# Kernel optimization log

Hardware: AMD Instinct MI355X
Metric: run time of the kernel (lower is better)

Reference implementation:

```python
import jax, jax.numpy as jnp
import numpy as np

B, N, D, K = 32, 196, 1024, 512  # batch, tokens (14x14), feature dim, prototypes
EPS = 1e-8  # torch F.cosine_similarity default eps


def setup_inputs() -> dict:
    key = jax.random.key(0)
    ks = jax.random.split(key, 8)
    z = jax.random.normal(ks[0], (B, N, D), jnp.float32)
    prototypes = jax.random.normal(ks[1], (K, D), jnp.float32)  # nn.Parameter(randn)
    gate_w = jax.random.normal(ks[2], (2 * D, D), jnp.float32) * 0.02  # Linear(2D->D), stored [in,out]
    gate_b = jnp.zeros((D,), jnp.float32)
    dec_w = jax.random.normal(ks[3], (D, 7 * 7 * 512), jnp.float32) * 0.02
    dec_b = jnp.zeros((7 * 7 * 512,), jnp.float32)
    ct1_w = jax.random.normal(ks[4], (512, 256, 4, 4), jnp.float32) * 0.02  # torch [in,out,kh,kw]
    ct1_b = jnp.zeros((256,), jnp.float32)
    ct2_w = jax.random.normal(ks[5], (256, 3, 4, 4), jnp.float32) * 0.02
    ct2_b = jnp.zeros((3,), jnp.float32)
    return dict(z=z, prototypes=prototypes, gate_w=gate_w, gate_b=gate_b,
                dec_w=dec_w, dec_b=dec_b, ct1_w=ct1_w, ct1_b=ct1_b,
                ct2_w=ct2_w, ct2_b=ct2_b)


def _conv_transpose(x, w, b):
    # ConvTranspose2d(k=4, stride=2, pad=1) == conv with lhs_dilation=2,
    # padding k-1-pad=2, spatially-flipped kernel, torch weight layout [in,out,kh,kw] -> IOHW.
    wf = jnp.flip(w, (2, 3))
    y = jax.lax.conv_general_dilated(
        x, wf, window_strides=(1, 1), padding=((2, 2), (2, 2)),
        lhs_dilation=(2, 2), dimension_numbers=("NCHW", "IOHW", "NCHW"))
    return y + b[None, :, None, None]


def reference(z, prototypes, gate_w, gate_b, dec_w, dec_b, ct1_w, ct1_b, ct2_w, ct2_b):
    # MemoryBank: cosine similarity of every token against every prototype
    zn = jnp.linalg.norm(z, axis=-1, keepdims=True)            # [B,N,1]
    pn = jnp.linalg.norm(prototypes, axis=-1)                  # [K]
    dots = jnp.einsum('bnd,kd->bnk', z, prototypes)            # [B,N,K]
    sim = dots / jnp.maximum(zn * pn[None, None, :], EPS)
    attn = jax.nn.softmax(sim, axis=-1)                        # [B,N,K]
    z_hat = jnp.einsum('bnk,kd->bnd', attn, prototypes)        # [B,N,D]
    # GatedFusion: sigmoid gate over concat(z, z_hat)
    gate = jax.nn.sigmoid(jnp.concatenate([z, z_hat], axis=-1) @ gate_w + gate_b)
    z_fused = gate * z + (1.0 - gate) * z_hat                  # [B,N,D]
    # Decoder (original reshape is shape-inconsistent; pool tokens -> [B,D])
    pooled = z_fused.mean(axis=1)                              # [B,D]
    h = (pooled @ dec_w + dec_b).reshape(-1, 512, 7, 7)
    h = jax.nn.relu(_conv_transpose(h, ct1_w, ct1_b))          # [B,256,14,14]
    x_recon = _conv_transpose(h, ct2_w, ct2_b)                 # [B,3,28,28]
    return x_recon, attn
```

## Files before the change

### kernel.cpp

```cpp
#include <hip/hip_runtime.h>
#include <cstdint>
#include <cstddef>
#include <cmath>

#define EPS_COS 1e-8f

typedef unsigned short u16;
typedef __attribute__((ext_vector_type(8))) short short8v;
typedef __attribute__((ext_vector_type(4))) short short4v;
typedef __attribute__((ext_vector_type(4))) float f32x4;

__device__ __forceinline__ u16 f2bf(float x) {
    unsigned int u = __float_as_uint(x);
    return (u16)((u + 0x7FFFu + ((u >> 16) & 1u)) >> 16);
}
__device__ __forceinline__ float bf2f(u16 h) {
    return __uint_as_float(((unsigned int)h) << 16);
}

__global__ __launch_bounds__(256) void norm_cvt_kernel(const float* __restrict__ src,
                                                       u16* __restrict__ dst, int dstStride,
                                                       float* __restrict__ norms) {
    int r = blockIdx.x;
    int t = threadIdx.x;
    const float4 v = *reinterpret_cast<const float4*>(&src[(size_t)r * 1024 + t * 4]);
    short4v o;
    o[0] = f2bf(v.x); o[1] = f2bf(v.y); o[2] = f2bf(v.z); o[3] = f2bf(v.w);
    *reinterpret_cast<short4v*>(&dst[(size_t)r * dstStride + t * 4]) = o;
    float ss = v.x * v.x + v.y * v.y + v.z * v.z + v.w * v.w;
#pragma unroll
    for (int off = 32; off > 0; off >>= 1) ss += __shfl_down(ss, off);
    __shared__ float red[4];
    int wave = t >> 6, lane = t & 63;
    if (lane == 0) red[wave] = ss;
    __syncthreads();
    if (t == 0) norms[r] = sqrtf(red[0] + red[1] + red[2] + red[3]);
}

__global__ __launch_bounds__(256) void transpose_cvt_kernel(const float* __restrict__ src,
                                                            u16* __restrict__ dst,
                                                            int R, int C) {
    __shared__ float tile[64][65];
    int c0 = blockIdx.x * 64, r0 = blockIdx.y * 64;
    int t = threadIdx.x;
#pragma unroll
    for (int j = 0; j < 16; ++j) {
        int idx = j * 256 + t;
        int r = idx >> 6, c = idx & 63;
        tile[r][c] = src[(size_t)(r0 + r) * C + c0 + c];
    }
    __syncthreads();
#pragma unroll
    for (int j = 0; j < 16; ++j) {
        int idx = j * 256 + t;
        int c = idx >> 6, r = idx & 63;
        dst[(size_t)(c0 + c) * R + r0 + r] = f2bf(tile[r][c]);
    }
}

__global__ __launch_bounds__(256) void prep_kernel(u16* __restrict__ hp,
                                                   const float* __restrict__ ct1w,
                                                   u16* __restrict__ wt,
                                                   const float* __restrict__ ct2w,
                                                   u16* __restrict__ wpad,
                                                   float* __restrict__ pooled) {
    int idx = blockIdx.x * 256 + threadIdx.x;
    if (idx < 165888) {
        short8v zv = {0, 0, 0, 0, 0, 0, 0, 0};
        *reinterpret_cast<short8v*>(hp + (size_t)idx * 8) = zv;
    } else if (idx < 165888 + 131072) {
        int i = idx - 165888;
        int oc = i & 255, ic = i >> 8;
        float v[16];
#pragma unroll
        for (int j = 0; j < 16; ++j) v[j] = ct1w[(size_t)i * 16 + j];
#pragma unroll
        for (int pp = 0; pp < 4; ++pp) {
            int py = pp >> 1, px = pp & 1;
#pragma unroll
            for (int tap = 0; tap < 4; ++tap) {
                int ty = tap >> 1, tx = tap & 1;
                int ky = (1 - py) + 2 * ty;
                int kx = (1 - px) + 2 * tx;
                wt[((size_t)(pp * 256 + oc)) * 2048 + ic * 4 + tap] = f2bf(v[ky * 4 + kx]);
            }
        }
    } else if (idx < 165888 + 131072 + 16384) {
        int i = idx - 165888 - 131072;
        int ic = i & 255;
        int col = i >> 8;
        float v = 0.0f;
        if (col < 48) {
            int kx = col & 3, ky = (col >> 2) & 3, oc = col >> 4;
            v = ct2w[((size_t)ic * 3 + oc) * 16 + ky * 4 + kx];
        }
        wpad[i] = f2bf(v);
    } else {
        int i = idx - 165888 - 131072 - 16384;
        *reinterpret_cast<f32x4*>(pooled + (size_t)i * 4) = (f32x4){0.f, 0.f, 0.f, 0.f};
    }
}

template <int FM, int FN, int EPI, bool SWZ>
__global__ __launch_bounds__(256) void mfma_gemm_kernel(
    const u16* __restrict__ A, int sA, size_t zsA,
    const u16* __restrict__ B, int sB, size_t zsB,
    int M, int N, int K,
    float* __restrict__ Cf,
    u16* __restrict__ Cb, int sCb,
    const float* __restrict__ bias,
    const u16* __restrict__ zbf,
    const u16* __restrict__ zhbf, int szh,
    float* __restrict__ outf) {
    constexpr int BM = FM * 32, BN = FN * 32;
    constexpr int NA = BM / 32;
    constexpr int NB = BN / 32;
    __shared__ __align__(16) u16 As[BM * 64];
    __shared__ __align__(16) u16 Bs[BN * 64];
    int bx = blockIdx.x, by = blockIdx.y;
    if (SWZ) {
        int gx = gridDim.x;
        int nwg = gx * gridDim.y;
        int lb = by * gx + bx;
        int flat = (lb & 7) * (nwg >> 3) + (lb >> 3);
        bx = flat % gx;
        by = flat / gx;
    }
    A += (size_t)blockIdx.z * zsA;
    B += (size_t)blockIdx.z * zsB;
    const int t = threadIdx.x;
    const int lane = t & 63;
    const int wid = t >> 6;
    const int wm = wid >> 1, wn = wid & 1;
    const int m0 = bx * BM, n0 = by * BN;
    const int g = lane >> 4, lr = lane & 15;

    f32x4 acc[FM][FN];
#pragma unroll
    for (int i = 0; i < FM; ++i)
#pragma unroll
        for (int j = 0; j < FN; ++j) acc[i][j] = (f32x4){0.f, 0.f, 0.f, 0.f};

    short8v ra[NA], rb[NB];
#pragma unroll
    for (int j = 0; j < NA; ++j) {
        int c = j * 256 + t, row = c >> 3, ck = c & 7;
        ra[j] = *reinterpret_cast<const short8v*>(A + (size_t)(m0 + row) * sA + ck * 8);
    }
#pragma unroll
    for (int j = 0; j < NB; ++j) {
        int c = j * 256 + t, row = c >> 3, ck = c & 7;
        rb[j] = *reinterpret_cast<const short8v*>(B + (size_t)(n0 + row) * sB + ck * 8);
    }

    for (int k0 = 0; k0 < K; k0 += 64) {
        __syncthreads();
#pragma unroll
        for (int j = 0; j < NA; ++j) {
            int c = j * 256 + t, row = c >> 3, ck = c & 7;
            *reinterpret_cast<short8v*>(As + row * 64 + ((ck ^ (row & 7)) << 3)) = ra[j];
        }
#pragma unroll
        for (int j = 0; j < NB; ++j) {
            int c = j * 256 + t, row = c >> 3, ck = c & 7;
            *reinterpret_cast<short8v*>(Bs + row * 64 + ((ck ^ (row & 7)) << 3)) = rb[j];
        }
        __syncthreads();
        if (k0 + 64 < K) {
#pragma unroll
            for (int j = 0; j < NA; ++j) {
                int c = j * 256 + t, row = c >> 3, ck = c & 7;
                ra[j] = *reinterpret_cast<const short8v*>(A + (size_t)(m0 + row) * sA + k0 + 64 + ck * 8);
            }
#pragma unroll
            for (int j = 0; j < NB; ++j) {
                int c = j * 256 + t, row = c >> 3, ck = c & 7;
                rb[j] = *reinterpret_cast<const short8v*>(B + (size_t)(n0 + row) * sB + k0 + 64 + ck * 8);
            }
        }
#pragma unroll
        for (int kk = 0; kk < 2; ++kk) {
            short8v af[FM], bfr[FN];
#pragma unroll
            for (int fm = 0; fm < FM; ++fm) {
                int row = wm * (FM * 16) + fm * 16 + lr;
                int rc = (kk * 4 + g) ^ (row & 7);
                af[fm] = *reinterpret_cast<const short8v*>(As + row * 64 + rc * 8);
            }
#pragma unroll
            for (int fn = 0; fn < FN; ++fn) {
                int col = wn * (FN * 16) + fn * 16 + lr;
                int rc = (kk * 4 + g) ^ (col & 7);
                bfr[fn] = *reinterpret_cast<const short8v*>(Bs + col * 64 + rc * 8);
            }
#pragma unroll
            for (int fm = 0; fm < FM; ++fm)
#pragma unroll
                for (int fn = 0; fn < FN; ++fn)
                    acc[fm][fn] = __builtin_amdgcn_mfma_f32_16x16x32_bf16(
                        af[fm], bfr[fn], acc[fm][fn], 0, 0, 0);
        }
    }

    if (EPI == 2) {
#pragma unroll
        for (int fn = 0; fn < FN; ++fn) {
            int col = n0 + wn * (FN * 16) + fn * 16 + lr;
            int base = m0 + wm * (FM * 16) + g * 4;
            int b0 = base / 196;
            float p0 = 0.f, p1 = 0.f;
#pragma unroll
            for (int fm = 0; fm < FM; ++fm) {
#pragma unroll
                for (int r = 0; r < 4; ++r) {
                    int row = base + fm * 16 + r;
                    float v = acc[fm][fn][r];
                    float gs = 1.0f / (1.0f + __expf(-(v + bias[col])));
                    float zv = bf2f(zbf[(size_t)row * szh + col]);
                    float zh = bf2f(zhbf[(size_t)row * szh + col]);
                    float fused = gs * zv + (1.0f - gs) * zh;
                    bool same = (row / 196) == b0;
                    p0 += same ? fused : 0.f;
                    p1 += same ? 0.f : fused;
                }
            }
            atomicAdd(&outf[(size_t)b0 * 1024 + col], p0);
            if (p1 != 0.f) atomicAdd(&outf[(size_t)(b0 + 1) * 1024 + col], p1);
        }
    } else {
#pragma unroll
        for (int fm = 0; fm < FM; ++fm) {
#pragma unroll
            for (int fn = 0; fn < FN; ++fn) {
#pragma unroll
                for (int r = 0; r < 4; ++r) {
                    int row = m0 + wm * (FM * 16) + fm * 16 + g * 4 + r;
                    int col = n0 + wn * (FN * 16) + fn * 16 + lr;
                    float v = acc[fm][fn][r];
                    if (EPI == 0) {
                        Cf[(size_t)row * N + col] = v;
                    } else if (EPI == 1) {
                        Cb[(size_t)row * sCb + col] = f2bf(v);
                    } else {
                        if (row < 1568) {
                            float vv = fmaxf(v + bias[col], 0.0f);
                            int bb = row / 49, ss = row - bb * 49;
                            Cb[(((size_t)bb * 4 + blockIdx.z) * 49 + ss) * 256 + col] = f2bf(vv);
                        }
                    }
                }
            }
        }
    }
}

__global__ __launch_bounds__(256) void softmax_kernel(const float* __restrict__ dots,
                                                      const float* __restrict__ zn,
                                                      const float* __restrict__ pn,
                                                      float* __restrict__ attn,
                                                      u16* __restrict__ attn_bf) {
    int m = blockIdx.x;
    int t = threadIdx.x;
    float zm = zn[m];
    float d0 = dots[(size_t)m * 512 + t];
    float d1 = dots[(size_t)m * 512 + t + 256];
    float v0 = d0 / fmaxf(zm * pn[t], EPS_COS);
    float v1 = d1 / fmaxf(zm * pn[t + 256], EPS_COS);
    float mx = fmaxf(v0, v1);
#pragma unroll
    for (int off = 32; off > 0; off >>= 1) mx = fmaxf(mx, __shfl_down(mx, off));
    __shared__ float red[8];
    int wave = t >> 6, lane = t & 63;
    if (lane == 0) red[wave] = mx;
    __syncthreads();
    if (t == 0) red[4] = fmaxf(fmaxf(red[0], red[1]), fmaxf(red[2], red[3]));
    __syncthreads();
    mx = red[4];
    float e0 = expf(v0 - mx), e1 = expf(v1 - mx);
    float s = e0 + e1;
#pragma unroll
    for (int off = 32; off > 0; off >>= 1) s += __shfl_down(s, off);
    if (lane == 0) red[wave] = s;
    __syncthreads();
    if (t == 0) red[5] = 1.0f / (red[0] + red[1] + red[2] + red[3]);
    __syncthreads();
    float r = red[5];
    float a0 = e0 * r, a1 = e1 * r;
    attn[(size_t)m * 512 + t] = a0;
    attn[(size_t)m * 512 + t + 256] = a1;
    attn_bf[(size_t)m * 512 + t] = f2bf(a0);
    attn_bf[(size_t)m * 512 + t + 256] = f2bf(a1);
}

#define DEC_KC 64
__global__ __launch_bounds__(256) void dec_split_kernel(const float* __restrict__ pooled,
                                                        const float* __restrict__ dec_w,
                                                        float* __restrict__ partial) {
    const int t = threadIdx.x;
    const int lane = t & 63;
    const int wv = t >> 6;
    const int c = blockIdx.x * 256 + lane * 4;
    const int kc = blockIdx.y;
    __shared__ float pl[32][DEC_KC];
    for (int i = t; i < 32 * DEC_KC; i += 256) {
        int b = i >> 6, kk = i & (DEC_KC - 1);
        pl[b][kk] = pooled[(size_t)b * 1024 + kc * DEC_KC + kk] * (1.0f / 196.0f);
    }
    __syncthreads();
    f32x4 acc[8];
#pragma unroll
    for (int j = 0; j < 8; ++j) acc[j] = (f32x4){0.f, 0.f, 0.f, 0.f};
    const float* wp = dec_w + (size_t)(kc * DEC_KC) * 25088 + c;
#pragma unroll 8
    for (int k = 0; k < DEC_KC; ++k) {
        f32x4 w4 = *reinterpret_cast<const f32x4*>(wp + (size_t)k * 25088);
#pragma unroll
        for (int j = 0; j < 8; ++j) {
            float pv = pl[wv * 8 + j][k];
            acc[j].x = fmaf(pv, w4.x, acc[j].x);
            acc[j].y = fmaf(pv, w4.y, acc[j].y);
            acc[j].z = fmaf(pv, w4.z, acc[j].z);
            acc[j].w = fmaf(pv, w4.w, acc[j].w);
        }
    }
#pragma unroll
    for (int j = 0; j < 8; ++j) {
        int b = wv * 8 + j;
        *reinterpret_cast<f32x4*>(partial + ((size_t)kc * 32 + b) * 25088 + c) = acc[j];
    }
}

__global__ __launch_bounds__(256) void dec_reduce_kernel(const float* __restrict__ partial,
                                                         const float* __restrict__ dec_b,
                                                         u16* __restrict__ hp) {
    int c = blockIdx.x * 256 + threadIdx.x;
    int b = blockIdx.y;
    float s = dec_b[c];
#pragma unroll
    for (int kc = 0; kc < 16; ++kc)
        s += partial[((size_t)kc * 32 + b) * 25088 + c];
    int ic = c / 49, sp = c - ic * 49;
    int sy = sp / 7, sx = sp - sy * 7;
    hp[((size_t)b * 512 + ic) * 81 + (sy + 1) * 9 + sx + 1] = f2bf(s);
}

__global__ __launch_bounds__(256) void im2col_kernel(const u16* __restrict__ hp,
                                                     u16* __restrict__ A) {
    int idx = blockIdx.x * 256 + threadIdx.x;
    int k8 = idx & 255;
    int pr = idx >> 8;
    int p = pr / 1600;
    int row = pr - p * 1600;
    short8v o = {0, 0, 0, 0, 0, 0, 0, 0};
    if (row < 1568) {
        int b = row / 49, s = row - b * 49;
        int sy = s / 7, sx = s - sy * 7;
        int r0 = sy + (p >> 1) + 1;
        int c0 = sx + (p & 1) + 1;
        int ic0 = k8 * 2;
        const u16* hb = hp + ((size_t)b * 512 + ic0) * 81;
#pragma unroll
        for (int j = 0; j < 2; ++j) {
            o[j * 4 + 0] = hb[r0 * 9 + c0];
            o[j * 4 + 1] = hb[r0 * 9 + c0 - 1];
            o[j * 4 + 2] = hb[(r0 - 1) * 9 + c0];
            o[j * 4 + 3] = hb[(r0 - 1) * 9 + c0 - 1];
            hb += 81;
        }
    }
    *reinterpret_cast<short8v*>(A + (size_t)idx * 8) = o;
}

__global__ __launch_bounds__(256) void convt2_gather_kernel(const float* __restrict__ G,
                                                            const float* __restrict__ bias,
                                                            float* __restrict__ out) {
    int o = blockIdx.x * 256 + threadIdx.x;
    int ox = o % 28;
    int oy = (o / 28) % 28;
    int oc = (o / 784) % 3;
    int b = o / 2352;
    int by = (oy + 1) >> 1, bx = (ox + 1) >> 1;
    float acc = bias[oc];
#pragma unroll
    for (int ty = 0; ty < 2; ++ty) {
        int iy = by - ty;
        if ((unsigned)iy >= 14u) continue;
#pragma unroll
        for (int tx = 0; tx < 2; ++tx) {
            int ix = bx - tx;
            if ((unsigned)ix >= 14u) continue;
            int p = (iy & 1) * 2 + (ix & 1);
            int row = ((b * 4 + p) * 49) + (iy >> 1) * 7 + (ix >> 1);
            int ky = oy + 1 - 2 * iy, kx = ox + 1 - 2 * ix;
            acc += G[(size_t)row * 64 + oc * 16 + ky * 4 + kx];
        }
    }
    out[o] = acc;
}

extern "C" void kernel_launch(void* const* d_in, const int* in_sizes, int n_in,
                              void* d_out, int out_size, void* d_ws, size_t ws_size,
                              hipStream_t stream) {
    const float* z      = (const float*)d_in[0];
    const float* protos = (const float*)d_in[1];
    const float* gate_w = (const float*)d_in[2];
    const float* gate_b = (const float*)d_in[3];
    const float* dec_w  = (const float*)d_in[4];
    const float* dec_b  = (const float*)d_in[5];
    const float* ct1_w  = (const float*)d_in[6];
    const float* ct1_b  = (const float*)d_in[7];
    const float* ct2_w  = (const float*)d_in[8];
    const float* ct2_b  = (const float*)d_in[9];

    float* xout = (float*)d_out;
    float* attn = xout + 75264;

    float* w = (float*)d_ws;
    float* pn        = w;
    float* zn        = w + 512;
    float* pooled    = w + 6784;
    u16*   wt1bf     = (u16*)(w + 51840);
    u16*   protos_bf = (u16*)(w + 1100416);
    u16*   protosT   = (u16*)(w + 1362560);
    u16*   gwT       = (u16*)(w + 1624704);
    u16*   attn_bf   = (u16*)(w + 2673280);
    u16*   Abig      = (u16*)(w + 4278912);
    u16*   A_cls     = (u16*)(w + 2673280);
    float* dots      = w + 10701440;
    float* partial   = w + 4278912;
    u16*   h2cb      = (u16*)(w + 11364992);
    u16*   hp        = (u16*)(w + 17123968);
    float* G         = w + 17787520;
    u16*   wpad      = (u16*)(w + 18188928);

    prep_kernel<<<1256, 256, 0, stream>>>(hp, ct1_w, wt1bf, ct2_w, wpad, pooled);
    norm_cvt_kernel<<<6272, 256, 0, stream>>>(z, Abig, 2048, zn);
    norm_cvt_kernel<<<512, 256, 0, stream>>>(protos, protos_bf, 1024, pn);
    transpose_cvt_kernel<<<dim3(16, 8), 256, 0, stream>>>(protos, protosT, 512, 1024);
    transpose_cvt_kernel<<<dim3(16, 32), 256, 0, stream>>>(gate_w, gwT, 2048, 1024);
    mfma_gemm_kernel<2, 4, 0, true><<<dim3(98, 4), 256, 0, stream>>>(
        Abig, 2048, 0, protos_bf, 1024, 0, 6272, 512, 1024,
        dots, nullptr, 0, nullptr, nullptr, nullptr, 0, nullptr);
    softmax_kernel<<<6272, 256, 0, stream>>>(dots, zn, pn, attn, attn_bf);
    mfma_gemm_kernel<4, 4, 1, true><<<dim3(49, 8), 256, 0, stream>>>(
        attn_bf, 512, 0, protosT, 512, 0, 6272, 1024, 512,
        nullptr, Abig + 1024, 2048, nullptr, nullptr, nullptr, 0, nullptr);
    mfma_gemm_kernel<4, 4, 2, true><<<dim3(49, 8), 256, 0, stream>>>(
        Abig, 2048, 0, gwT, 2048, 0, 6272, 1024, 2048,
        nullptr, nullptr, 0, gate_b, Abig, Abig + 1024, 2048, pooled);
    dec_split_kernel<<<dim3(98, 16), 256, 0, stream>>>(pooled, dec_w, partial);
    dec_reduce_kernel<<<dim3(98, 32), 256, 0, stream>>>(partial, dec_b, hp);
    im2col_kernel<<<6400, 256, 0, stream>>>(hp, A_cls);
    mfma_gemm_kernel<2, 2, 3, false><<<dim3(25, 4, 4), 256, 0, stream>>>(
        A_cls, 2048, (size_t)1600 * 2048, wt1bf, 2048, (size_t)256 * 2048,
        1600, 256, 2048, nullptr, h2cb, 0, ct1_b, nullptr, nullptr, 0, nullptr);
    mfma_gemm_kernel<2, 2, 0, false><<<dim3(98, 1), 256, 0, stream>>>(
        h2cb, 256, 0, wpad, 256, 0, 6272, 64, 256,
        G, nullptr, 0, nullptr, nullptr, nullptr, 0, nullptr);
    convt2_gather_kernel<<<294, 256, 0, stream>>>(G, ct2_b, xout);
}
```

Baseline: 207.8 us.

## Store decoder partials in bf16, batch weight loads, shrink GEMM tiles for more blocks

The decoder split-K kernel now issues eight weight loads per iteration before the FMAs, which raises memory-level parallelism. It writes its partial sums as bf16 instead of fp32, halving partial-buffer traffic, and the reduce kernel handles two columns per thread. Several MFMA GEMM launches switch to smaller M tiles with proportionally larger grids so more blocks occupy the CUs. Rounding partial sums to bf16 before the reduction adds numerical error.

```diff
diff --git a/kernel.cpp b/kernel.cpp
--- a/kernel.cpp
+++ b/kernel.cpp
@@ -295,7 +295,7 @@
 #define DEC_KC 64
 __global__ __launch_bounds__(256) void dec_split_kernel(const float* __restrict__ pooled,
                                                         const float* __restrict__ dec_w,
-                                                        float* __restrict__ partial) {
+                                                        u16* __restrict__ partial) {
     const int t = threadIdx.x;
     const int lane = t & 63;
     const int wv = t >> 6;
@@ -311,37 +311,56 @@
 #pragma unroll
     for (int j = 0; j < 8; ++j) acc[j] = (f32x4){0.f, 0.f, 0.f, 0.f};
     const float* wp = dec_w + (size_t)(kc * DEC_KC) * 25088 + c;
-#pragma unroll 8
-    for (int k = 0; k < DEC_KC; ++k) {
-        f32x4 w4 = *reinterpret_cast<const f32x4*>(wp + (size_t)k * 25088);
-#pragma unroll
-        for (int j = 0; j < 8; ++j) {
-            float pv = pl[wv * 8 + j][k];
-            acc[j].x = fmaf(pv, w4.x, acc[j].x);
-            acc[j].y = fmaf(pv, w4.y, acc[j].y);
-            acc[j].z = fmaf(pv, w4.z, acc[j].z);
-            acc[j].w = fmaf(pv, w4.w, acc[j].w);
+#pragma unroll 1
+    for (int k = 0; k < DEC_KC; k += 8) {
+        f32x4 wv8[8];
+#pragma unroll
+        for (int q = 0; q < 8; ++q)
+            wv8[q] = *reinterpret_cast<const f32x4*>(wp + (size_t)(k + q) * 25088);
+#pragma unroll
+        for (int q = 0; q < 8; ++q) {
+#pragma unroll
+            for (int j = 0; j < 8; ++j) {
+                float pv = pl[wv * 8 + j][k + q];
+                acc[j].x = fmaf(pv, wv8[q].x, acc[j].x);
+                acc[j].y = fmaf(pv, wv8[q].y, acc[j].y);
+                acc[j].z = fmaf(pv, wv8[q].z, acc[j].z);
+                acc[j].w = fmaf(pv, wv8[q].w, acc[j].w);
+            }
         }
     }
 #pragma unroll
     for (int j = 0; j < 8; ++j) {
         int b = wv * 8 + j;
-        *reinterpret_cast<f32x4*>(partial + ((size_t)kc * 32 + b) * 25088 + c) = acc[j];
-    }
-}
-
-__global__ __launch_bounds__(256) void dec_reduce_kernel(const float* __restrict__ partial,
+        short4v o;
+        o[0] = f2bf(acc[j].x); o[1] = f2bf(acc[j].y);
+        o[2] = f2bf(acc[j].z); o[3] = f2bf(acc[j].w);
+        *reinterpret_cast<short4v*>(partial + ((size_t)kc * 32 + b) * 25088 + c) = o;
+    }
+}
+
+__global__ __launch_bounds__(256) void dec_reduce_kernel(const u16* __restrict__ partial,
                                                          const float* __restrict__ dec_b,
                                                          u16* __restrict__ hp) {
-    int c = blockIdx.x * 256 + threadIdx.x;
+    int c = (blockIdx.x * 256 + threadIdx.x) * 2;
     int b = blockIdx.y;
-    float s = dec_b[c];
-#pragma unroll
-    for (int kc = 0; kc < 16; ++kc)
-        s += partial[((size_t)kc * 32 + b) * 25088 + c];
-    int ic = c / 49, sp = c - ic * 49;
-    int sy = sp / 7, sx = sp - sy * 7;
-    hp[((size_t)b * 512 + ic) * 81 + (sy + 1) * 9 + sx + 1] = f2bf(s);
+    float2 bb = *reinterpret_cast<const float2*>(&dec_b[c]);
+    float s0 = bb.x, s1 = bb.y;
+#pragma unroll
+    for (int kc = 0; kc < 16; ++kc) {
+        unsigned int v = *reinterpret_cast<const unsigned int*>(
+            partial + ((size_t)kc * 32 + b) * 25088 + c);
+        s0 += bf2f((u16)(v & 0xffffu));
+        s1 += bf2f((u16)(v >> 16));
+    }
+#pragma unroll
+    for (int q = 0; q < 2; ++q) {
+        int cc = c + q;
+        float s = q ? s1 : s0;
+        int ic = cc / 49, sp = cc - ic * 49;
+        int sy = sp / 7, sx = sp - sy * 7;
+        hp[((size_t)b * 512 + ic) * 81 + (sy + 1) * 9 + sx + 1] = f2bf(s);
+    }
 }
 
 __global__ __launch_bounds__(256) void im2col_kernel(const u16* __restrict__ hp,
@@ -427,7 +446,7 @@
     u16*   Abig      = (u16*)(w + 4278912);
     u16*   A_cls     = (u16*)(w + 2673280);
     float* dots      = w + 10701440;
-    float* partial   = w + 4278912;
+    u16*   partial   = (u16*)(w + 4278912);
     u16*   h2cb      = (u16*)(w + 11364992);
     u16*   hp        = (u16*)(w + 17123968);
     float* G         = w + 17787520;
@@ -442,19 +461,19 @@
         Abig, 2048, 0, protos_bf, 1024, 0, 6272, 512, 1024,
         dots, nullptr, 0, nullptr, nullptr, nullptr, 0, nullptr);
     softmax_kernel<<<6272, 256, 0, stream>>>(dots, zn, pn, attn, attn_bf);
-    mfma_gemm_kernel<4, 4, 1, true><<<dim3(49, 8), 256, 0, stream>>>(
+    mfma_gemm_kernel<2, 4, 1, true><<<dim3(98, 8), 256, 0, stream>>>(
         attn_bf, 512, 0, protosT, 512, 0, 6272, 1024, 512,
         nullptr, Abig + 1024, 2048, nullptr, nullptr, nullptr, 0, nullptr);
-    mfma_gemm_kernel<4, 4, 2, true><<<dim3(49, 8), 256, 0, stream>>>(
+    mfma_gemm_kernel<2, 4, 2, true><<<dim3(98, 8), 256, 0, stream>>>(
         Abig, 2048, 0, gwT, 2048, 0, 6272, 1024, 2048,
         nullptr, nullptr, 0, gate_b, Abig, Abig + 1024, 2048, pooled);
     dec_split_kernel<<<dim3(98, 16), 256, 0, stream>>>(pooled, dec_w, partial);
-    dec_reduce_kernel<<<dim3(98, 32), 256, 0, stream>>>(partial, dec_b, hp);
+    dec_reduce_kernel<<<dim3(49, 32), 256, 0, stream>>>(partial, dec_b, hp);
     im2col_kernel<<<6400, 256, 0, stream>>>(hp, A_cls);
-    mfma_gemm_kernel<2, 2, 3, false><<<dim3(25, 4, 4), 256, 0, stream>>>(
+    mfma_gemm_kernel<1, 2, 3, false><<<dim3(50, 4, 4), 256, 0, stream>>>(
         A_cls, 2048, (size_t)1600 * 2048, wt1bf, 2048, (size_t)256 * 2048,
         1600, 256, 2048, nullptr, h2cb, 0, ct1_b, nullptr, nullptr, 0, nullptr);
-    mfma_gemm_kernel<2, 2, 0, false><<<dim3(98, 1), 256, 0, stream>>>(
+    mfma_gemm_kernel<1, 2, 0, false><<<dim3(196, 1), 256, 0, stream>>>(
         h2cb, 256, 0, wpad, 256, 0, 6272, 64, 256,
         G, nullptr, 0, nullptr, nullptr, nullptr, 0, nullptr);
     convt2_gather_kernel<<<294, 256, 0, stream>>>(G, ct2_b, xout);
```

New measurement: 217.0 us. 4.4% more time.
